# Performance work log

Hardware: AMD Instinct MI355X
Metric: run time of the kernel (lower is better)

## Reference

```python
import jax, jax.numpy as jnp
import numpy as np

D_MODEL = 1024
N_HEADS = 16
D_K = D_MODEL // N_HEADS
D_FF = 4096
EPS = 1e-5
NEG_INF = -1e9


def entmax15(x, axis=-1):
    """Exact alpha-entmax with alpha=1.5 (sort-based), along `axis`."""
    x = x / 2.0
    x = x - jnp.max(x, axis=axis, keepdims=True)  # shift-invariant, for stability
    zs = -jnp.sort(-x, axis=axis)                 # descending sort
    n = x.shape[axis]
    shape = [1] * x.ndim
    shape[axis] = n
    k = jnp.arange(1, n + 1, dtype=x.dtype).reshape(shape)
    mean = jnp.cumsum(zs, axis=axis) / k
    mean_sq = jnp.cumsum(zs * zs, axis=axis) / k
    ss = k * (mean_sq - mean * mean)
    delta = (1.0 - ss) / k
    tau = mean - jnp.sqrt(jnp.maximum(delta, 0.0))
    support = (tau <= zs).astype(jnp.int32)
    support_size = jnp.sum(support, axis=axis, keepdims=True)  # >= 1 always
    tau_star = jnp.take_along_axis(tau, support_size - 1, axis=axis)
    p = jnp.maximum(x - tau_star, 0.0)
    return p * p


def layer_norm(x, g, b):
    m = jnp.mean(x, axis=-1, keepdims=True)
    v = jnp.mean((x - m) ** 2, axis=-1, keepdims=True)
    return (x - m) / jnp.sqrt(v + EPS) * g + b


def setup_inputs() -> dict:
    key = jax.random.key(0)
    ks = jax.random.split(key, 16)
    B, S, D = 2, 1024, D_MODEL
    s = 0.02
    return {
        "x": jax.random.normal(ks[0], (B, S, D), jnp.float32),
        "mask": jnp.ones((B, S, S), jnp.bool_),
        "Wq": jax.random.normal(ks[1], (D, D), jnp.float32) * s,
        "bq": jnp.zeros((D,), jnp.float32),
        "Wk": jax.random.normal(ks[2], (D, D), jnp.float32) * s,
        "bk": jnp.zeros((D,), jnp.float32),
        "Wv": jax.random.normal(ks[3], (D, D), jnp.float32) * s,
        "bv": jnp.zeros((D,), jnp.float32),
        "Wo": jax.random.normal(ks[4], (D, D), jnp.float32) * s,
        "bo": jnp.zeros((D,), jnp.float32),
        "W1": jax.random.normal(ks[5], (D, D_FF), jnp.float32) * s,
        "b1": jnp.zeros((D_FF,), jnp.float32),
        "W2": jax.random.normal(ks[6], (D_FF, D), jnp.float32) * s,
        "b2": jnp.zeros((D,), jnp.float32),
        "g1": jnp.ones((D,), jnp.float32),
        "be1": jnp.zeros((D,), jnp.float32),
        "g2": jnp.ones((D,), jnp.float32),
        "be2": jnp.zeros((D,), jnp.float32),
    }


def reference(x, mask, Wq, bq, Wk, bk, Wv, bv, Wo, bo, W1, b1, W2, b2, g1, be1, g2, be2):
    B, S, D = x.shape
    # --- pre-norm + multi-head entmax-1.5 attention ---
    h = layer_norm(x, g1, be1)
    def split_heads(t):  # [B,S,D] -> [B,H,S,dk]
        return t.reshape(B, S, N_HEADS, D_K).transpose(0, 2, 1, 3)
    q = split_heads(h @ Wq + bq)
    k = split_heads(h @ Wk + bk)
    v = split_heads(h @ Wv + bv)
    scores = jnp.einsum('bhqd,bhkd->bhqk', q, k) / jnp.sqrt(jnp.float32(D_K))
    scores = jnp.where(mask[:, None, :, :], scores, NEG_INF)
    attn = entmax15(scores, axis=-1)          # sparse (entmax-1.5) normalization
    ctx = jnp.einsum('bhqk,bhkd->bhqd', attn, v)
    ctx = ctx.transpose(0, 2, 1, 3).reshape(B, S, D)
    x = x + (ctx @ Wo + bo)                    # residual (dropout = identity, eval)
    # --- pre-norm FFN ---
    h = layer_norm(x, g2, be2)
    ff = jax.nn.relu(h @ W1 + b1) @ W2 + b2
    return x + ff
```

## Files before the change

### kernel.cpp

```cpp
#include <hip/hip_runtime.h>
#include <hip/hip_bf16.h>
#include <stdint.h>

#define DM   1024
#define DFF  4096
#define NB   2
#define SEQ  1024
#define NH   16
#define DKH  64
#define NROWS (NB*SEQ)

typedef unsigned short u16;
typedef __attribute__((ext_vector_type(8))) short bf16x8;
typedef __attribute__((ext_vector_type(8))) unsigned short u16x8;
typedef __attribute__((ext_vector_type(4))) float f32x4;

static const long SQ2 = (long)SEQ * SEQ;

__device__ __forceinline__ u16 f2bf(float f) {
  unsigned int b = __float_as_uint(f);
  b += 0x7FFFu + ((b >> 16) & 1u);
  return (u16)(b >> 16);
}
__device__ __forceinline__ float bf2f(u16 u) {
  return __uint_as_float(((unsigned int)u) << 16);
}

__device__ __forceinline__ void gload_lds16(const void* g, void* l) {
  __builtin_amdgcn_global_load_lds(
      (__attribute__((address_space(1))) void*)g,
      (__attribute__((address_space(3))) void*)l, 16, 0, 0);
}

__global__ __launch_bounds__(256) void ln_kernel(const float* __restrict__ x,
    const float* __restrict__ g, const float* __restrict__ b,
    u16* __restrict__ o) {
  const int row = blockIdx.x;
  const int tid = threadIdx.x;
  const float4 v = ((const float4*)(x + (long)row * DM))[tid];
  float s  = v.x + v.y + v.z + v.w;
  float sq = v.x*v.x + v.y*v.y + v.z*v.z + v.w*v.w;
#pragma unroll
  for (int off = 32; off; off >>= 1) {
    s  += __shfl_xor(s,  off, 64);
    sq += __shfl_xor(sq, off, 64);
  }
  __shared__ float sm1[4], sm2[4];
  const int wid = tid >> 6;
  if ((tid & 63) == 0) { sm1[wid] = s; sm2[wid] = sq; }
  __syncthreads();
  s  = sm1[0] + sm1[1] + sm1[2] + sm1[3];
  sq = sm2[0] + sm2[1] + sm2[2] + sm2[3];
  const float mean = s * (1.0f / DM);
  const float var  = sq * (1.0f / DM) - mean * mean;
  const float rstd = rsqrtf(var + 1e-5f);
  const float4 g4 = ((const float4*)g)[tid];
  const float4 b4 = ((const float4*)b)[tid];
  ushort4 ov;
  ov.x = f2bf((v.x - mean) * rstd * g4.x + b4.x);
  ov.y = f2bf((v.y - mean) * rstd * g4.y + b4.y);
  ov.z = f2bf((v.z - mean) * rstd * g4.z + b4.z);
  ov.w = f2bf((v.w - mean) * rstd * g4.w + b4.w);
  ((ushort4*)(o + (long)row * DM))[tid] = ov;
}

__global__ __launch_bounds__(256) void tcast_kernel(const float* __restrict__ in,
    u16* __restrict__ out, int R, int C) {
  __shared__ float t[32][33];
  const int bx = blockIdx.x * 32;
  const int by = blockIdx.y * 32;
  const int tx = threadIdx.x & 31;
  const int ty4 = (threadIdx.x >> 5) * 4;
#pragma unroll
  for (int j = 0; j < 4; ++j)
    t[ty4 + j][tx] = in[(long)(by + ty4 + j) * C + bx + tx];
  __syncthreads();
#pragma unroll
  for (int j = 0; j < 4; ++j)
    out[(long)(bx + ty4 + j) * R + by + tx] = f2bf(t[tx][ty4 + j]);
}

template <int BM, int BN, int WMW, int WNW, int CMODE, bool RELU>
__global__ __launch_bounds__(256) void mm_kernel(
    const u16* __restrict__ A, int lda, long sAb, long sAh,
    const u16* __restrict__ B, int ldb, long sBb, long sBh,
    const float* __restrict__ bias, const float* __restrict__ bias2,
    const float* __restrict__ bias3, const float* __restrict__ res,
    void* __restrict__ Cv, int ldc, long sCb, long sCh,
    int K) {
  constexpr int WTM = BM / WMW;
  constexpr int WN  = BN / WNW;
  constexpr int FM  = WTM / 16;
  constexpr int FN  = WN / 16;
  constexpr int APW = BM / 64;
  constexpr int BPW = BN / 64;

  __shared__ __align__(16) u16 As[BM * 32];
  __shared__ __align__(16) u16 Bs[BN * 32];

  const int z = blockIdx.z;
  const long zb = z >> 4, zh = z & 15;
  A += zb * sAb + zh * sAh;
  B += zb * sBb + zh * sBh;
  const long coff = zb * sCb + zh * sCh;

  const int tid  = threadIdx.x;
  const int wid  = tid >> 6;
  const int lane = tid & 63;
  const int wm   = wid / WNW;
  const int wn   = wid % WNW;
  const int lrow = lane >> 2;
  const int lk8  = (lane & 3) * 8;
  const int l15  = lane & 15;
  const int l16  = lane >> 4;

  const int m0 = blockIdx.y * BM;
  const int n0 = blockIdx.x * BN;

  f32x4 acc[FM][FN] = {};

  for (int k0 = 0; k0 < K; k0 += 32) {
#pragma unroll
    for (int c = 0; c < APW; ++c) {
      const int ch = wid * APW + c;
      gload_lds16(A + (long)(m0 + ch * 16 + lrow) * lda + (k0 + lk8),
                  &As[ch * 512]);
    }
#pragma unroll
    for (int c = 0; c < BPW; ++c) {
      const int ch = wid * BPW + c;
      gload_lds16(B + (long)(n0 + ch * 16 + lrow) * ldb + (k0 + lk8),
                  &Bs[ch * 512]);
    }
    __syncthreads();

    bf16x8 af[FM], bfr[FN];
    const int ab = (wm * WTM + l15) * 32 + l16 * 8;
    const int bb = (wn * WN + l15) * 32 + l16 * 8;
#pragma unroll
    for (int i = 0; i < FM; ++i) af[i]  = *(const bf16x8*)&As[ab + i * 512];
#pragma unroll
    for (int j = 0; j < FN; ++j) bfr[j] = *(const bf16x8*)&Bs[bb + j * 512];
#pragma unroll
    for (int i = 0; i < FM; ++i)
#pragma unroll
      for (int j = 0; j < FN; ++j)
        acc[i][j] = __builtin_amdgcn_mfma_f32_16x16x32_bf16(
            af[i], bfr[j], acc[i][j], 0, 0, 0);
    __syncthreads();
  }

#pragma unroll
  for (int i = 0; i < FM; ++i) {
    const int row0 = m0 + wm * WTM + i * 16 + l16 * 4;
#pragma unroll
    for (int j = 0; j < FN; ++j) {
      const int col = n0 + wn * WN + j * 16 + l15;
      if (CMODE == 3) {
        const int seg = col >> 10;
        if (seg == 2) {
          const int cc = col - 2048;
          const float bv = bias3[cc];
          const long ob = (long)(row0 >> 10) * ((long)NH * DKH * SEQ)
                        + (long)cc * SEQ + (row0 & 1023);
          ushort4 o;
          o.x = f2bf(acc[i][j][0] + bv);
          o.y = f2bf(acc[i][j][1] + bv);
          o.z = f2bf(acc[i][j][2] + bv);
          o.w = f2bf(acc[i][j][3] + bv);
          *(ushort4*)&((u16*)Cv)[4194304 + ob] = o;
        } else {
          const int cc = col - (seg << 10);
          const float bv = seg ? bias2[cc] : bias[cc];
          u16* dst = (u16*)Cv + (long)seg * 2097152;
#pragma unroll
          for (int r = 0; r < 4; ++r)
            dst[(long)(row0 + r) * DM + cc] = f2bf(acc[i][j][r] + bv);
        }
      } else {
        const float bv = bias ? bias[col] : 0.0f;
#pragma unroll
        for (int r = 0; r < 4; ++r) {
          const long m = row0 + r;
          float v = acc[i][j][r] + bv;
          if (res)  v += res[m * ldc + col];
          if (RELU) v = fmaxf(v, 0.0f);
          if (CMODE == 0) ((float*)Cv)[coff + m * ldc + col] = v;
          else            ((u16*)Cv)[coff + m * ldc + col] = f2bf(v);
        }
      }
    }
  }
}

__global__ __launch_bounds__(256, 2) void attn_kernel(
    const u16* __restrict__ q_bf, const u16* __restrict__ k_bf,
    const u16* __restrict__ vT, u16* __restrict__ ctx_bf) {
  __shared__ __align__(16) u16 sc[32 * 1032];
  __shared__ __align__(16) u16 Qs[4 * 512];
  __shared__ __align__(16) u16 Ks[8 * 512];

  const int qb  = blockIdx.x;
  const int bh  = blockIdx.y;
  const int b   = bh >> 4, h = bh & 15;
  const int tid = threadIdx.x;
  const int wid = tid >> 6;
  const int lane = tid & 63;
  const int l15 = lane & 15, l16 = lane >> 4;
  const int lrow = lane >> 2, lk8 = (lane & 3) * 8;

  const long qrow0 = (long)b * SEQ + qb * 32;
  const long krow0 = (long)b * SEQ;
  const int qt = wid >> 1;
  const int ah = wid & 1;

  gload_lds16(q_bf + (qrow0 + (wid >> 1) * 16 + lrow) * DM
                   + h * 64 + (wid & 1) * 32 + lk8,
              &Qs[wid * 512]);

  for (int c = 0; c < 16; ++c) {
#pragma unroll
    for (int i = 0; i < 2; ++i) {
      const int ch = wid * 2 + i;
      gload_lds16(k_bf + (krow0 + c * 64 + (ch >> 1) * 16 + lrow) * DM
                       + h * 64 + (ch & 1) * 32 + lk8,
                  &Ks[ch * 512]);
    }
    __syncthreads();
#pragma unroll
    for (int a2 = 0; a2 < 2; ++a2) {
      const int a = ah * 2 + a2;
      f32x4 acc = {};
#pragma unroll
      for (int kc = 0; kc < 2; ++kc) {
        bf16x8 af = *(const bf16x8*)&Ks[(a * 2 + kc) * 512 + l15 * 32 + l16 * 8];
        bf16x8 bq = *(const bf16x8*)&Qs[(qt * 2 + kc) * 512 + l15 * 32 + l16 * 8];
        acc = __builtin_amdgcn_mfma_f32_16x16x32_bf16(af, bq, acc, 0, 0, 0);
      }
      ushort4 o;
      o.x = f2bf(acc[0]); o.y = f2bf(acc[1]);
      o.z = f2bf(acc[2]); o.w = f2bf(acc[3]);
      *(ushort4*)&sc[(qt * 16 + l15) * 1032 + c * 64 + a * 16 + l16 * 4] = o;
    }
    __syncthreads();
  }

  {
    const int g = lane >> 3;
    const int j = lane & 7;
    u16* rowp = &sc[(wid * 8 + g) * 1032];

    float xs[128];
#pragma unroll
    for (int t = 0; t < 16; ++t) {
      u16x8 v = *(const u16x8*)&rowp[t * 64 + j * 8];
#pragma unroll
      for (int e = 0; e < 8; ++e)
        xs[t * 8 + e] = bf2f(v[e]) * (1.0f / 16.0f);
    }

    float mx = xs[0];
#pragma unroll
    for (int i = 1; i < 128; ++i) mx = fmaxf(mx, xs[i]);
    mx = fmaxf(mx, __shfl_xor(mx, 1, 64));
    mx = fmaxf(mx, __shfl_xor(mx, 2, 64));
    mx = fmaxf(mx, __shfl_xor(mx, 4, 64));
#pragma unroll
    for (int i = 0; i < 128; ++i) xs[i] -= mx;

    float lo = -1.0f, hi = 0.0f, tau = -1.0f;
    for (int it = 0; it < 16; ++it) {
      float cc = 0.f, sx = 0.f, sx2 = 0.f;
#pragma unroll
      for (int i = 0; i < 128; ++i) {
        const bool in = xs[i] > tau;
        const float xv = in ? xs[i] : 0.f;
        cc += in ? 1.f : 0.f;
        sx += xv;
        sx2 = fmaf(xv, xv, sx2);
      }
      cc += __shfl_xor(cc, 1, 64); sx += __shfl_xor(sx, 1, 64); sx2 += __shfl_xor(sx2, 1, 64);
      cc += __shfl_xor(cc, 2, 64); sx += __shfl_xor(sx, 2, 64); sx2 += __shfl_xor(sx2, 2, 64);
      cc += __shfl_xor(cc, 4, 64); sx += __shfl_xor(sx, 4, 64); sx2 += __shfl_xor(sx2, 4, 64);
      const float f = sx2 - 2.0f * tau * sx + cc * tau * tau - 1.0f;
      const bool conv = (fabsf(f) < 1e-4f) || ((hi - lo) < 2e-6f);
      if (__all(conv)) break;
      lo = (!conv && f > 0.0f) ? tau : lo;
      hi = (!conv && f <= 0.0f) ? tau : hi;
      const float rk  = 1.0f / cc;
      const float m   = sx * rk;
      const float msq = sx2 * rk;
      const float delta = m * m - msq + rk;
      float prop = m - sqrtf(fmaxf(delta, 0.0f));
      if (!(prop > lo && prop < hi)) prop = 0.5f * (lo + hi);
      tau = conv ? tau : prop;
    }

#pragma unroll
    for (int t = 0; t < 16; ++t) {
      u16x8 o;
#pragma unroll
      for (int e = 0; e < 8; ++e) {
        const float d = fmaxf(xs[t * 8 + e] - tau, 0.f);
        o[e] = f2bf(d * d);
      }
      *(u16x8*)&rowp[t * 64 + j * 8] = o;
    }
  }
  __syncthreads();

  const int dh = wid & 1;
  const u16* vbase = vT + ((long)b * (NH * DKH) + h * 64) * SEQ;
  f32x4 pacc[2] = {};
#pragma unroll 4
  for (int ks = 0; ks < 32; ++ks) {
    bf16x8 af = *(const bf16x8*)&sc[(qt * 16 + l15) * 1032 + ks * 32 + l16 * 8];
#pragma unroll
    for (int dt2 = 0; dt2 < 2; ++dt2) {
      const int dt = dh * 2 + dt2;
      bf16x8 bv = *(const bf16x8*)&vbase[(long)(dt * 16 + l15) * SEQ
                                         + ks * 32 + l16 * 8];
      pacc[dt2] = __builtin_amdgcn_mfma_f32_16x16x32_bf16(af, bv, pacc[dt2], 0, 0, 0);
    }
  }
#pragma unroll
  for (int dt2 = 0; dt2 < 2; ++dt2) {
    const int d = (dh * 2 + dt2) * 16 + l15;
#pragma unroll
    for (int r = 0; r < 4; ++r) {
      const long q = qrow0 + qt * 16 + l16 * 4 + r;
      ctx_bf[q * DM + h * 64 + d] = f2bf(pacc[dt2][r]);
    }
  }
}

extern "C" void kernel_launch(void* const* d_in, const int* in_sizes, int n_in,
                              void* d_out, int out_size, void* d_ws, size_t ws_size,
                              hipStream_t stream) {
  const float* x   = (const float*)d_in[0];
  const float* Wq  = (const float*)d_in[2];
  const float* bq  = (const float*)d_in[3];
  const float* Wk  = (const float*)d_in[4];
  const float* bk  = (const float*)d_in[5];
  const float* Wv  = (const float*)d_in[6];
  const float* bv  = (const float*)d_in[7];
  const float* Wo  = (const float*)d_in[8];
  const float* bo  = (const float*)d_in[9];
  const float* W1  = (const float*)d_in[10];
  const float* b1  = (const float*)d_in[11];
  const float* W2  = (const float*)d_in[12];
  const float* b2  = (const float*)d_in[13];
  const float* g1  = (const float*)d_in[14];
  const float* be1 = (const float*)d_in[15];
  const float* g2  = (const float*)d_in[16];
  const float* be2 = (const float*)d_in[17];
  float* out = (float*)d_out;

  char* w = (char*)d_ws;
  u16*   h_bf  = (u16*)w;            w += (long)NROWS * DM * 2;
  u16*   q_bf  = (u16*)w;            w += (long)NROWS * DM * 2;
  u16*   k_bf  = (u16*)w;            w += (long)NROWS * DM * 2;
  u16*   vT    = (u16*)w;            w += (long)NROWS * DM * 2;
  u16*   ctx_bf= (u16*)w;            w += (long)NROWS * DM * 2;
  float* x2    = (float*)w;          w += (long)NROWS * DM * 4;
  u16*   h2_bf = (u16*)w;            w += (long)NROWS * DM * 2;
  u16*   ff_bf = (u16*)w;            w += (long)NROWS * DFF * 2;
  u16*   WqkvT = (u16*)w;            w += (long)3 * DM * DM * 2;
  u16*   WoT   = (u16*)w;            w += (long)DM * DM * 2;
  u16*   W1T   = (u16*)w;            w += (long)DM * DFF * 2;
  u16*   W2T   = (u16*)w;            w += (long)DM * DFF * 2;

  tcast_kernel<<<dim3(32, 32),  256, 0, stream>>>(Wq, WqkvT,                DM, DM);
  tcast_kernel<<<dim3(32, 32),  256, 0, stream>>>(Wk, WqkvT + 1024 * 1024,  DM, DM);
  tcast_kernel<<<dim3(32, 32),  256, 0, stream>>>(Wv, WqkvT + 2048 * 1024,  DM, DM);
  tcast_kernel<<<dim3(32, 32),  256, 0, stream>>>(Wo, WoT, DM, DM);
  tcast_kernel<<<dim3(128, 32), 256, 0, stream>>>(W1, W1T, DM, DFF);
  tcast_kernel<<<dim3(32, 128), 256, 0, stream>>>(W2, W2T, DFF, DM);

  ln_kernel<<<NROWS, 256, 0, stream>>>(x, g1, be1, h_bf);

  mm_kernel<128, 128, 2, 2, 3, false><<<dim3(24, 16, 1), 256, 0, stream>>>(
      h_bf, DM, 0, 0, WqkvT, DM, 0, 0, bq, bk, bv, nullptr,
      q_bf, DM, 0, 0, DM);

  attn_kernel<<<dim3(32, 32), 256, 0, stream>>>(q_bf, k_bf, vT, ctx_bf);

  mm_kernel<64, 64, 2, 2, 0, false><<<dim3(16, 32, 1), 256, 0, stream>>>(
      ctx_bf, DM, 0, 0, WoT, DM, 0, 0, bo, nullptr, nullptr, x,
      x2, DM, 0, 0, DM);

  ln_kernel<<<NROWS, 256, 0, stream>>>(x2, g2, be2, h2_bf);

  mm_kernel<128, 128, 2, 2, 1, true><<<dim3(32, 16, 1), 256, 0, stream>>>(
      h2_bf, DM, 0, 0, W1T, DM, 0, 0, b1, nullptr, nullptr, nullptr,
      ff_bf, DFF, 0, 0, DM);

  mm_kernel<64, 64, 2, 2, 0, false><<<dim3(16, 32, 1), 256, 0, stream>>>(
      ff_bf, DFF, 0, 0, W2T, DFF, 0, 0, b2, nullptr, nullptr, x2,
      out, DM, 0, 0, DFF);
}
```

Baseline: 365.1 us.

## Halve attention query tile, double-buffer K loads, drop per-chunk barriers

The attention kernel now processes 16 query rows per block instead of 32, doubling the grid and raising the launch-bounds occupancy target to 4 blocks per CU with smaller LDS. K tiles are double-buffered with waits on per-wave load counters instead of two block barriers per chunk. Entmax rows are split across 16 lanes, and the PV product uses two interleaved accumulators. The trade-off is that K and V are re-read by twice as many blocks, and correctness now relies on each wave reading only the K rows it loaded itself.

```diff
diff --git a/kernel.cpp b/kernel.cpp
--- a/kernel.cpp
+++ b/kernel.cpp
@@ -193,12 +193,12 @@
   }
 }
 
-__global__ __launch_bounds__(256, 2) void attn_kernel(
+__global__ __launch_bounds__(256, 4) void attn_kernel(
     const u16* __restrict__ q_bf, const u16* __restrict__ k_bf,
     const u16* __restrict__ vT, u16* __restrict__ ctx_bf) {
-  __shared__ __align__(16) u16 sc[32 * 1032];
-  __shared__ __align__(16) u16 Qs[4 * 512];
-  __shared__ __align__(16) u16 Ks[8 * 512];
+  __shared__ __align__(16) u16 sc[16 * 1032];
+  __shared__ __align__(16) u16 Qs[2 * 512];
+  __shared__ __align__(16) u16 Ks[2][8 * 512];
 
   const int qb  = blockIdx.x;
   const int bh  = blockIdx.y;
@@ -209,51 +209,57 @@
   const int l15 = lane & 15, l16 = lane >> 4;
   const int lrow = lane >> 2, lk8 = (lane & 3) * 8;
 
-  const long qrow0 = (long)b * SEQ + qb * 32;
+  const long qrow0 = (long)b * SEQ + qb * 16;
   const long krow0 = (long)b * SEQ;
-  const int qt = wid >> 1;
-  const int ah = wid & 1;
-
-  gload_lds16(q_bf + (qrow0 + (wid >> 1) * 16 + lrow) * DM
-                   + h * 64 + (wid & 1) * 32 + lk8,
-              &Qs[wid * 512]);
+
+  if (wid < 2)
+    gload_lds16(q_bf + (qrow0 + lrow) * DM + h * 64 + wid * 32 + lk8,
+                &Qs[wid * 512]);
+
+#define STAGE_K(c, buf)                                                     \
+  {                                                                         \
+    _Pragma("unroll")                                                       \
+    for (int i_ = 0; i_ < 2; ++i_) {                                        \
+      gload_lds16(k_bf + (krow0 + (c) * 64 + wid * 16 + lrow) * DM          \
+                       + h * 64 + i_ * 32 + lk8,                            \
+                  &Ks[buf][(wid * 2 + i_) * 512]);                          \
+    }                                                                       \
+  }
+
+  STAGE_K(0, 0);
+  __syncthreads();
 
   for (int c = 0; c < 16; ++c) {
-#pragma unroll
-    for (int i = 0; i < 2; ++i) {
-      const int ch = wid * 2 + i;
-      gload_lds16(k_bf + (krow0 + c * 64 + (ch >> 1) * 16 + lrow) * DM
-                       + h * 64 + (ch & 1) * 32 + lk8,
-                  &Ks[ch * 512]);
-    }
-    __syncthreads();
-#pragma unroll
-    for (int a2 = 0; a2 < 2; ++a2) {
-      const int a = ah * 2 + a2;
-      f32x4 acc = {};
-#pragma unroll
-      for (int kc = 0; kc < 2; ++kc) {
-        bf16x8 af = *(const bf16x8*)&Ks[(a * 2 + kc) * 512 + l15 * 32 + l16 * 8];
-        bf16x8 bq = *(const bf16x8*)&Qs[(qt * 2 + kc) * 512 + l15 * 32 + l16 * 8];
-        acc = __builtin_amdgcn_mfma_f32_16x16x32_bf16(af, bq, acc, 0, 0, 0);
-      }
-      ushort4 o;
-      o.x = f2bf(acc[0]); o.y = f2bf(acc[1]);
-      o.z = f2bf(acc[2]); o.w = f2bf(acc[3]);
-      *(ushort4*)&sc[(qt * 16 + l15) * 1032 + c * 64 + a * 16 + l16 * 4] = o;
-    }
-    __syncthreads();
-  }
+    const int cur = c & 1;
+    if (c < 15) {
+      STAGE_K(c + 1, cur ^ 1);
+      asm volatile("s_waitcnt vmcnt(2)" ::: "memory");
+    } else {
+      asm volatile("s_waitcnt vmcnt(0)" ::: "memory");
+    }
+    f32x4 acc = {};
+#pragma unroll
+    for (int kc = 0; kc < 2; ++kc) {
+      bf16x8 af = *(const bf16x8*)&Ks[cur][(wid * 2 + kc) * 512 + l15 * 32 + l16 * 8];
+      bf16x8 bq = *(const bf16x8*)&Qs[kc * 512 + l15 * 32 + l16 * 8];
+      acc = __builtin_amdgcn_mfma_f32_16x16x32_bf16(af, bq, acc, 0, 0, 0);
+    }
+    ushort4 o;
+    o.x = f2bf(acc[0]); o.y = f2bf(acc[1]);
+    o.z = f2bf(acc[2]); o.w = f2bf(acc[3]);
+    *(ushort4*)&sc[l15 * 1032 + c * 64 + wid * 16 + l16 * 4] = o;
+  }
+  __syncthreads();
 
   {
-    const int g = lane >> 3;
-    const int j = lane & 7;
-    u16* rowp = &sc[(wid * 8 + g) * 1032];
-
-    float xs[128];
-#pragma unroll
-    for (int t = 0; t < 16; ++t) {
-      u16x8 v = *(const u16x8*)&rowp[t * 64 + j * 8];
+    const int g = lane >> 4;
+    const int j = lane & 15;
+    u16* rowp = &sc[(wid * 4 + g) * 1032];
+
+    float xs[64];
+#pragma unroll
+    for (int t = 0; t < 8; ++t) {
+      u16x8 v = *(const u16x8*)&rowp[t * 128 + j * 8];
 #pragma unroll
       for (int e = 0; e < 8; ++e)
         xs[t * 8 + e] = bf2f(v[e]) * (1.0f / 16.0f);
@@ -261,27 +267,31 @@
 
     float mx = xs[0];
 #pragma unroll
-    for (int i = 1; i < 128; ++i) mx = fmaxf(mx, xs[i]);
+    for (int i = 1; i < 64; ++i) mx = fmaxf(mx, xs[i]);
     mx = fmaxf(mx, __shfl_xor(mx, 1, 64));
     mx = fmaxf(mx, __shfl_xor(mx, 2, 64));
     mx = fmaxf(mx, __shfl_xor(mx, 4, 64));
-#pragma unroll
-    for (int i = 0; i < 128; ++i) xs[i] -= mx;
+    mx = fmaxf(mx, __shfl_xor(mx, 8, 64));
+#pragma unroll
+    for (int i = 0; i < 64; ++i) xs[i] -= mx;
 
     float lo = -1.0f, hi = 0.0f, tau = -1.0f;
     for (int it = 0; it < 16; ++it) {
       float cc = 0.f, sx = 0.f, sx2 = 0.f;
 #pragma unroll
-      for (int i = 0; i < 128; ++i) {
+      for (int i = 0; i < 64; ++i) {
         const bool in = xs[i] > tau;
         const float xv = in ? xs[i] : 0.f;
         cc += in ? 1.f : 0.f;
         sx += xv;
         sx2 = fmaf(xv, xv, sx2);
       }
-      cc += __shfl_xor(cc, 1, 64); sx += __shfl_xor(sx, 1, 64); sx2 += __shfl_xor(sx2, 1, 64);
-      cc += __shfl_xor(cc, 2, 64); sx += __shfl_xor(sx, 2, 64); sx2 += __shfl_xor(sx2, 2, 64);
-      cc += __shfl_xor(cc, 4, 64); sx += __shfl_xor(sx, 4, 64); sx2 += __shfl_xor(sx2, 4, 64);
+#pragma unroll
+      for (int off = 1; off <= 8; off <<= 1) {
+        cc  += __shfl_xor(cc,  off, 64);
+        sx  += __shfl_xor(sx,  off, 64);
+        sx2 += __shfl_xor(sx2, off, 64);
+      }
       const float f = sx2 - 2.0f * tau * sx + cc * tau * tau - 1.0f;
       const bool conv = (fabsf(f) < 1e-4f) || ((hi - lo) < 2e-6f);
       if (__all(conv)) break;
@@ -297,41 +307,35 @@
     }
 
 #pragma unroll
-    for (int t = 0; t < 16; ++t) {
+    for (int t = 0; t < 8; ++t) {
       u16x8 o;
 #pragma unroll
       for (int e = 0; e < 8; ++e) {
         const float d = fmaxf(xs[t * 8 + e] - tau, 0.f);
         o[e] = f2bf(d * d);
       }
-      *(u16x8*)&rowp[t * 64 + j * 8] = o;
+      *(u16x8*)&rowp[t * 128 + j * 8] = o;
     }
   }
   __syncthreads();
 
-  const int dh = wid & 1;
-  const u16* vbase = vT + ((long)b * (NH * DKH) + h * 64) * SEQ;
-  f32x4 pacc[2] = {};
+  const u16* vbase = vT + ((long)b * (NH * DKH) + h * 64 + wid * 16) * SEQ;
+  f32x4 pacc0 = {}, pacc1 = {};
 #pragma unroll 4
-  for (int ks = 0; ks < 32; ++ks) {
-    bf16x8 af = *(const bf16x8*)&sc[(qt * 16 + l15) * 1032 + ks * 32 + l16 * 8];
-#pragma unroll
-    for (int dt2 = 0; dt2 < 2; ++dt2) {
-      const int dt = dh * 2 + dt2;
-      bf16x8 bv = *(const bf16x8*)&vbase[(long)(dt * 16 + l15) * SEQ
-                                         + ks * 32 + l16 * 8];
-      pacc[dt2] = __builtin_amdgcn_mfma_f32_16x16x32_bf16(af, bv, pacc[dt2], 0, 0, 0);
-    }
-  }
-#pragma unroll
-  for (int dt2 = 0; dt2 < 2; ++dt2) {
-    const int d = (dh * 2 + dt2) * 16 + l15;
-#pragma unroll
-    for (int r = 0; r < 4; ++r) {
-      const long q = qrow0 + qt * 16 + l16 * 4 + r;
-      ctx_bf[q * DM + h * 64 + d] = f2bf(pacc[dt2][r]);
-    }
-  }
+  for (int ks = 0; ks < 32; ks += 2) {
+    bf16x8 a0 = *(const bf16x8*)&sc[l15 * 1032 + ks * 32 + l16 * 8];
+    bf16x8 b0 = *(const bf16x8*)&vbase[(long)l15 * SEQ + ks * 32 + l16 * 8];
+    pacc0 = __builtin_amdgcn_mfma_f32_16x16x32_bf16(a0, b0, pacc0, 0, 0, 0);
+    bf16x8 a1 = *(const bf16x8*)&sc[l15 * 1032 + (ks + 1) * 32 + l16 * 8];
+    bf16x8 b1 = *(const bf16x8*)&vbase[(long)l15 * SEQ + (ks + 1) * 32 + l16 * 8];
+    pacc1 = __builtin_amdgcn_mfma_f32_16x16x32_bf16(a1, b1, pacc1, 0, 0, 0);
+  }
+#pragma unroll
+  for (int r = 0; r < 4; ++r) {
+    const long q = qrow0 + l16 * 4 + r;
+    ctx_bf[q * DM + h * 64 + wid * 16 + l15] = f2bf(pacc0[r] + pacc1[r]);
+  }
+#undef STAGE_K
 }
 
 extern "C" void kernel_launch(void* const* d_in, const int* in_sizes, int n_in,
@@ -383,7 +387,7 @@
       h_bf, DM, 0, 0, WqkvT, DM, 0, 0, bq, bk, bv, nullptr,
       q_bf, DM, 0, 0, DM);
 
-  attn_kernel<<<dim3(32, 32), 256, 0, stream>>>(q_bf, k_bf, vT, ctx_bf);
+  attn_kernel<<<dim3(64, 32), 256, 0, stream>>>(q_bf, k_bf, vT, ctx_bf);
 
   mm_kernel<64, 64, 2, 2, 0, false><<<dim3(16, 32, 1), 256, 0, stream>>>(
       ctx_bf, DM, 0, 0, WoT, DM, 0, 0, bo, nullptr, nullptr, x,
```

Result: faster. 350.7 us (-4.0%).
